# Kernel tuning notes

Hardware: AMD Instinct MI355X
Metric: run time of the kernel (lower is better)

The kernel has to match this reference:

```python
import jax, jax.numpy as jnp
import numpy as np

B, L, D = 256, 512, 768
ATTN_H, WIDTH_DIM = 1000, 20
BINS = jnp.array([1, 2, 3, 4, 5, 6, 7, 8, 12, 16, 20, 24, 32, 64, 128], dtype=jnp.int64)


def setup_inputs() -> dict:
    key = jax.random.key(0)
    ks = jax.random.split(key, 20)
    s = 0.02
    embeds = jax.random.normal(ks[0], (B, L, D), dtype=jnp.float32)
    spans = jnp.sort(jax.random.randint(ks[1], (B, 2), 0, L, dtype=jnp.int64), axis=1)
    inp = {
        "embeds": embeds,
        "spans": spans,
        # attention scorer: Linear(768,1000) -> LeakyReLU -> Linear(1000,1)
        "aw1": jax.random.normal(ks[2], (D, ATTN_H), dtype=jnp.float32) * s,
        "ab1": jnp.zeros((ATTN_H,), dtype=jnp.float32),
        "aw2": jax.random.normal(ks[3], (ATTN_H, 1), dtype=jnp.float32) * s,
        "ab2": jnp.zeros((1,), dtype=jnp.float32),
        # width embedding: [len(bins)+1 = 16, 20]
        "width_emb": jax.random.normal(ks[4], (16, WIDTH_DIM), dtype=jnp.float32) * s,
        # score MLP: 2324 -> 1024 -> 512 -> 256 -> 30
        "sw1": jax.random.normal(ks[5], (2324, 1024), dtype=jnp.float32) * s,
        "sb1": jnp.zeros((1024,), dtype=jnp.float32),
        "sw2": jax.random.normal(ks[6], (1024, 512), dtype=jnp.float32) * s,
        "sb2": jnp.zeros((512,), dtype=jnp.float32),
        "sw3": jax.random.normal(ks[7], (512, 256), dtype=jnp.float32) * s,
        "sb3": jnp.zeros((256,), dtype=jnp.float32),
        "sw4": jax.random.normal(ks[8], (256, 30), dtype=jnp.float32) * s,
        "sb4": jnp.zeros((30,), dtype=jnp.float32),
    }
    return inp


def reference(embeds, spans, aw1, ab1, aw2, ab2, width_emb,
              sw1, sb1, sw2, sb2, sw3, sb3, sw4, sb4):
    b, l, d = embeds.shape
    start, end = spans[:, 0], spans[:, 1]

    # gather start/end token embeds -> [B, 2*D]
    se = jnp.take_along_axis(embeds, spans[:, :, None], axis=1).reshape(b, 2 * d)

    # attention logits over all tokens: Linear -> LeakyReLU -> Linear
    h = jax.nn.leaky_relu(embeds @ aw1 + ab1)          # [B, L, 1000]
    attns = (h @ aw2 + ab2)[..., 0]                     # [B, L]

    # ragged per-span softmax pooling, vectorized via masking (inclusive span)
    cols = jnp.arange(l, dtype=spans.dtype)[None, :]
    mask = (cols >= start[:, None]) & (cols <= end[:, None])
    w = jax.nn.softmax(jnp.where(mask, attns, jnp.float32(-1e30)), axis=1)
    w = w * mask.astype(w.dtype)
    attn_embeds = jnp.einsum("bl,bld->bd", w, embeds)   # [B, D]

    # width bucket embedding
    widths = end - start + 1
    idx = jnp.sum(widths[:, None] > BINS[None, :], axis=1)
    wemb = width_emb[idx]                                # [B, 20]

    x = jnp.concatenate([se, attn_embeds, wemb], axis=1)  # [B, 2324]
    x = jax.nn.leaky_relu(x @ sw1 + sb1)
    x = jax.nn.leaky_relu(x @ sw2 + sb2)
    x = jax.nn.leaky_relu(x @ sw3 + sb3)
    return x @ sw4 + sb4                                  # [B, 30]
```

## Files before the change

### kernel.cpp

```cpp
#include <hip/hip_runtime.h>
#include <hip/hip_bf16.h>

#define B_   256
#define L_   512
#define D_   768
#define H_   1000
#define NPAD 1024
#define XDIM 2324
#define MAXPOS (B_*L_)

typedef _Float16 half8 __attribute__((ext_vector_type(8)));
typedef float    f32x4 __attribute__((ext_vector_type(4)));

__global__ __launch_bounds__(256) void scan_kernel(const int* __restrict__ spans,
                                                   int* __restrict__ meta) {
    int b = threadIdx.x;
    int s = spans[2 * b], e = spans[2 * b + 1];
    s = min(max(s, 0), L_ - 1);
    e = min(max(e, s), L_ - 1);
    int w = e - s + 1;
    __shared__ int sw[256];
    sw[b] = w;
    __syncthreads();
    for (int d = 1; d < 256; d <<= 1) {
        int v = 0;
        if (b >= d) v = sw[b - d];
        __syncthreads();
        if (b >= d) sw[b] += v;
        __syncthreads();
    }
    meta[b]       = sw[b] - w;
    meta[256 + b] = s;
    meta[512 + b] = e;
    if (b == 255) meta[768] = sw[255];
}

__global__ __launch_bounds__(256) void pos_fill(const int* __restrict__ meta,
                                                int* __restrict__ pos_list) {
    int b = blockIdx.x;
    int off = meta[b], start = meta[256 + b], end = meta[512 + b];
    int w = end - start + 1;
    for (int i = threadIdx.x; i < w; i += blockDim.x)
        pos_list[off + i] = (b << 16) | (start + i);
}

__global__ __launch_bounds__(256) void transpose_w(const float* __restrict__ aw1,
                                                   _Float16* __restrict__ WbT) {
    int k0 = blockIdx.x * 32, n0 = blockIdx.y * 32;
    int tx = threadIdx.x & 31, ty = threadIdx.x >> 5;
    __shared__ float T[32][33];
#pragma unroll
    for (int it = 0; it < 4; it++) {
        int k = k0 + ty + 8 * it;
        int n = n0 + tx;
        T[ty + 8 * it][tx] = (n < H_) ? aw1[(size_t)k * H_ + n] : 0.f;
    }
    __syncthreads();
#pragma unroll
    for (int it = 0; it < 4; it++) {
        int n = n0 + ty + 8 * it;
        WbT[(size_t)n * D_ + k0 + tx] = (_Float16)T[tx][ty + 8 * it];
    }
}

#define BM   128
#define BN   256
#define BKT  32
#define NKST (D_ / BKT)

#define GLD_LDS16(gsrc, ldst) \
    __builtin_amdgcn_global_load_lds((const __attribute__((address_space(1))) void*)(gsrc), \
                                     (__attribute__((address_space(3))) void*)(ldst), 16, 0, 0)

__global__ __launch_bounds__(512, 4) void attn_gemm_v4(
    const float* __restrict__ embeds, const _Float16* __restrict__ WbT,
    const float* __restrict__ ab1, const float* __restrict__ aw2,
    const int* __restrict__ pos_list, const int* __restrict__ meta,
    float* __restrict__ attns) {
    int npos = meta[768];
    int m0 = blockIdx.x * BM;
    if (m0 >= npos) return;
    int n0 = blockIdx.y * BN;
    int t = threadIdx.x;
    int lane = t & 63, w = t >> 6;
    int q = lane >> 4, l15 = lane & 15;
    int wr = w >> 2, wc = w & 3;

    __shared__ alignas(16) _Float16 As[2][BM][BKT];
    __shared__ alignas(16) _Float16 Bs[2][BN * BKT];
    __shared__ unsigned rowoff[BM];

    if (t < BM) {
        unsigned off = 0;
        int m = m0 + t;
        if (m < npos) {
            int p = pos_list[m];
            off = (unsigned)((p >> 16) * (L_ * D_) + (p & 0xffff) * D_);
        }
        rowoff[t] = off;
    }
    __syncthreads();

    const int arow = t >> 2;
    const int acol = (t & 3) * 8;
    const float* aptr = embeds + rowoff[arow] + acol;

    const _Float16* bptr = WbT + (size_t)(n0 + (t >> 2)) * D_ + (t & 3) * 8;

    float4 ar0, ar1;
    auto loadA = [&](int k0) {
        const float* p = aptr + k0;
        ar0 = *(const float4*)(p + 0);
        ar1 = *(const float4*)(p + 4);
    };
    auto writeA = [&](int bbuf) {
        half8 h0;
        h0[0] = (_Float16)ar0.x; h0[1] = (_Float16)ar0.y;
        h0[2] = (_Float16)ar0.z; h0[3] = (_Float16)ar0.w;
        h0[4] = (_Float16)ar1.x; h0[5] = (_Float16)ar1.y;
        h0[6] = (_Float16)ar1.z; h0[7] = (_Float16)ar1.w;
        *(half8*)&As[bbuf][arow][acol] = h0;
    };
    auto issueB = [&](int bbuf, int k0) {
        const _Float16* s0 = bptr + k0;
        _Float16* d0 = &Bs[bbuf][0] + w * 512;
        GLD_LDS16(s0, d0);
        const _Float16* s1 = s0 + (size_t)128 * D_;
        _Float16* d1 = d0 + 4096;
        GLD_LDS16(s1, d1);
    };

    f32x4 acc[4][4];
#pragma unroll
    for (int mi = 0; mi < 4; mi++)
#pragma unroll
        for (int ni = 0; ni < 4; ni++) acc[mi][ni] = (f32x4){0.f, 0.f, 0.f, 0.f};

    auto compute = [&](int bbuf) {
        half8 af[4], bf[4];
#pragma unroll
        for (int mi = 0; mi < 4; mi++)
            af[mi] = *(const half8*)&As[bbuf][wr * 64 + mi * 16 + l15][q * 8];
#pragma unroll
        for (int ni = 0; ni < 4; ni++)
            bf[ni] = *(const half8*)&Bs[bbuf][((wc * 64 + ni * 16 + l15) << 5) + q * 8];
#pragma unroll
        for (int mi = 0; mi < 4; mi++)
#pragma unroll
            for (int ni = 0; ni < 4; ni++)
                acc[mi][ni] = __builtin_amdgcn_mfma_f32_16x16x32_f16(
                    af[mi], bf[ni], acc[mi][ni], 0, 0, 0);
    };

    issueB(0, 0);
    loadA(0);
    writeA(0);
    __syncthreads();

    int buf = 0;
#pragma unroll 2
    for (int ks = 0; ks < NKST - 1; ks++) {
        int kn = (ks + 1) * BKT;
        issueB(buf ^ 1, kn);
        loadA(kn);
        compute(buf);
        writeA(buf ^ 1);
        __syncthreads();
        buf ^= 1;
    }
    compute(buf);

    int colb = n0 + wc * 64;
    float bj[4], aj[4];
#pragma unroll
    for (int ni = 0; ni < 4; ni++) {
        int col = colb + ni * 16 + l15;
        bool v = col < H_;
        bj[ni] = v ? ab1[col] : 0.f;
        aj[ni] = v ? aw2[col] : 0.f;
    }
#pragma unroll
    for (int mi = 0; mi < 4; mi++) {
#pragma unroll
        for (int r = 0; r < 4; r++) {
            float p = 0.f;
#pragma unroll
            for (int ni = 0; ni < 4; ni++) {
                float h = acc[mi][ni][r] + bj[ni];
                h = h > 0.f ? h : 0.01f * h;
                p += h * aj[ni];
            }
            p += __shfl_xor(p, 1);
            p += __shfl_xor(p, 2);
            p += __shfl_xor(p, 4);
            p += __shfl_xor(p, 8);
            if (l15 == 0) {
                int row = m0 + wr * 64 + mi * 16 + q * 4 + r;
                if (row < npos) atomicAdd(&attns[row], p);
            }
        }
    }
}

__global__ __launch_bounds__(256) void build_x(
    const float* __restrict__ embeds, const float* __restrict__ attns,
    const int* __restrict__ meta, const float* __restrict__ width_emb,
    float* __restrict__ x) {
    int b = blockIdx.x, s = blockIdx.y, t = threadIdx.x;
    int off = meta[b], start = meta[256 + b], end = meta[512 + b];
    int w = end - start + 1;
    __shared__ float sv[512];
    __shared__ float red[256];
    for (int i = t; i < w; i += 256) sv[i] = attns[off + i];
    __syncthreads();
    float m = -3.0e38f;
    for (int i = t; i < w; i += 256) m = fmaxf(m, sv[i]);
    red[t] = m;
    __syncthreads();
    for (int st = 128; st > 0; st >>= 1) {
        if (t < st) red[t] = fmaxf(red[t], red[t + st]);
        __syncthreads();
    }
    float mx = red[0];
    __syncthreads();
    float ssum = 0.f;
    for (int i = t; i < w; i += 256) {
        float e = __expf(sv[i] - mx);
        sv[i] = e;
        ssum += e;
    }
    red[t] = ssum;
    __syncthreads();
    for (int st = 128; st > 0; st >>= 1) {
        if (t < st) red[t] += red[t + st];
        __syncthreads();
    }
    float inv = 1.0f / red[0];
    __syncthreads();

    int dim = s * 256 + t;
    const float* base = embeds + ((size_t)b * L_ + start) * D_ + dim;
    float acc = 0.f;
    int i = 0;
    for (; i + 3 < w; i += 4) {
        float w0 = sv[i], w1 = sv[i + 1], w2 = sv[i + 2], w3 = sv[i + 3];
        const float* p = base + (size_t)i * D_;
        acc += w0 * p[0] + w1 * p[D_] + w2 * p[2 * D_] + w3 * p[3 * D_];
    }
    for (; i < w; i++) acc += sv[i] * base[(size_t)i * D_];

    float* xb = x + (size_t)b * XDIM;
    xb[1536 + dim] = acc * inv;
    xb[dim]        = base[0];
    xb[768 + dim]  = embeds[((size_t)b * L_ + end) * D_ + dim];
    if (s == 0 && t < 20) {
        const int bins[15] = {1, 2, 3, 4, 5, 6, 7, 8, 12, 16, 20, 24, 32, 64, 128};
        int idx = 0;
#pragma unroll
        for (int q2 = 0; q2 < 15; q2++) idx += (w > bins[q2]);
        xb[2304 + t] = width_emb[idx * 20 + t];
    }
}

__global__ __launch_bounds__(256) void mlp_gemm_sk(
    const float* __restrict__ A, const float* __restrict__ abias, int aleaky,
    const float* __restrict__ W, float* __restrict__ out,
    int M, int N, int K, int kchunk) {
    __shared__ float As[16][68];
    __shared__ float Ws[16][64];
    int t = threadIdx.x;
    int tx = t & 15, ty = t >> 4;
    int m0 = blockIdx.x * 64, n0 = blockIdx.y * 64;
    int ks = blockIdx.z * kchunk;
    int ke = min(ks + kchunk, K);
    if (ks >= ke) return;
    int ar = t >> 2, akc = (t & 3) * 4;
    int wk = t >> 4, wnc = (t & 15) * 4;
    bool n4 = ((N & 3) == 0);

    float acc[4][4];
#pragma unroll
    for (int i = 0; i < 4; i++)
#pragma unroll
        for (int j = 0; j < 4; j++) acc[i][j] = 0.f;

    auto loadA = [&](int k0) -> float4 {
        float4 r = make_float4(0.f, 0.f, 0.f, 0.f);
        int k = k0 + akc;
        if (k < ke) {
            r = *(const float4*)(A + (size_t)(m0 + ar) * K + k);
            if (abias) {
                r.x += abias[k];     r.y += abias[k + 1];
                r.z += abias[k + 2]; r.w += abias[k + 3];
                if (aleaky) {
                    r.x = r.x > 0.f ? r.x : 0.01f * r.x;
                    r.y = r.y > 0.f ? r.y : 0.01f * r.y;
                    r.z = r.z > 0.f ? r.z : 0.01f * r.z;
                    r.w = r.w > 0.f ? r.w : 0.01f * r.w;
                }
            }
        }
        return r;
    };
    auto loadW = [&](int k0) -> float4 {
        float4 r = make_float4(0.f, 0.f, 0.f, 0.f);
        int k = k0 + wk;
        if (k < ke) {
            int n = n0 + wnc;
            const float* p = W + (size_t)k * N + n;
            if (n4) {
                r = *(const float4*)p;
            } else {
                float tmp[4];
#pragma unroll
                for (int q2 = 0; q2 < 4; q2++)
                    tmp[q2] = (n + q2 < N) ? p[q2] : 0.f;
                r = make_float4(tmp[0], tmp[1], tmp[2], tmp[3]);
            }
        }
        return r;
    };

    float4 aR = loadA(ks), wR = loadW(ks);
    for (int k0 = ks; k0 < ke; k0 += 16) {
        As[akc + 0][ar] = aR.x;
        As[akc + 1][ar] = aR.y;
        As[akc + 2][ar] = aR.z;
        As[akc + 3][ar] = aR.w;
        *(float4*)&Ws[wk][wnc] = wR;
        __syncthreads();
        if (k0 + 16 < ke) { aR = loadA(k0 + 16); wR = loadW(k0 + 16); }
#pragma unroll
        for (int kk = 0; kk < 16; kk++) {
            float4 a = *(const float4*)&As[kk][ty * 4];
            float4 b = *(const float4*)&Ws[kk][tx * 4];
            float av[4] = {a.x, a.y, a.z, a.w};
            float bv[4] = {b.x, b.y, b.z, b.w};
#pragma unroll
            for (int i = 0; i < 4; i++)
#pragma unroll
                for (int j = 0; j < 4; j++) acc[i][j] += av[i] * bv[j];
        }
        __syncthreads();
    }
#pragma unroll
    for (int i = 0; i < 4; i++) {
#pragma unroll
        for (int j = 0; j < 4; j++) {
            int nn = n0 + tx * 4 + j;
            if (nn < N)
                atomicAdd(&out[(size_t)(m0 + ty * 4 + i) * N + nn], acc[i][j]);
        }
    }
}

__global__ __launch_bounds__(256) void bias_act(
    const float* __restrict__ src, const float* __restrict__ bias,
    float* __restrict__ dst, int total, int N, int leaky) {
    int i = blockIdx.x * 256 + threadIdx.x;
    int stride = gridDim.x * 256;
    for (; i < total; i += stride) {
        float v = src[i] + bias[i % N];
        if (leaky) v = v > 0.f ? v : 0.01f * v;
        dst[i] = v;
    }
}

extern "C" void kernel_launch(void* const* d_in, const int* in_sizes, int n_in,
                              void* d_out, int out_size, void* d_ws, size_t ws_size,
                              hipStream_t stream) {
    const float* embeds    = (const float*)d_in[0];
    const int*   spans     = (const int*)d_in[1];
    const float* aw1       = (const float*)d_in[2];
    const float* ab1       = (const float*)d_in[3];
    const float* aw2       = (const float*)d_in[4];
    const float* width_emb = (const float*)d_in[6];
    const float* sw1 = (const float*)d_in[7],  *sb1 = (const float*)d_in[8];
    const float* sw2 = (const float*)d_in[9],  *sb2 = (const float*)d_in[10];
    const float* sw3 = (const float*)d_in[11], *sb3 = (const float*)d_in[12];
    const float* sw4 = (const float*)d_in[13], *sb4 = (const float*)d_in[14];
    float* out = (float*)d_out;

    char* ws = (char*)d_ws;
    float*     attns    = (float*)ws;
    int*       pos_list = (int*)(ws + (size_t)MAXPOS * 4);
    int*       meta     = (int*)(ws + (size_t)MAXPOS * 8);
    _Float16*  WbT      = (_Float16*)(ws + (size_t)MAXPOS * 8 + 4096);
    float* x  = (float*)(ws + (size_t)MAXPOS * 8 + 4096 + (size_t)NPAD * D_ * 2);
    float* y1 = x + (size_t)B_ * XDIM;
    float* y2 = y1 + (size_t)B_ * 1024;
    float* y3 = y2 + (size_t)B_ * 512;
    float* y4 = y3 + (size_t)B_ * 256;
    size_t ybytes = ((size_t)B_ * (1024 + 512 + 256 + 30)) * 4;

    hipMemsetAsync(y1, 0, ybytes, stream);
    hipMemsetAsync(attns, 0, (size_t)MAXPOS * 4, stream);
    scan_kernel<<<1, 256, 0, stream>>>(spans, meta);
    pos_fill<<<B_, 256, 0, stream>>>(meta, pos_list);
    transpose_w<<<dim3(D_ / 32, NPAD / 32), 256, 0, stream>>>(aw1, WbT);
    attn_gemm_v4<<<dim3(MAXPOS / BM, NPAD / BN), 512, 0, stream>>>(
        embeds, WbT, ab1, aw2, pos_list, meta, attns);
    build_x<<<dim3(B_, 3), 256, 0, stream>>>(embeds, attns, meta, width_emb, x);

    mlp_gemm_sk<<<dim3(4, 16, 8), 256, 0, stream>>>(x,  nullptr, 0, sw1, y1, B_, 1024, XDIM, 292);
    mlp_gemm_sk<<<dim3(4, 8, 8), 256, 0, stream>>>(y1, sb1, 1, sw2, y2, B_, 512, 1024, 128);
    mlp_gemm_sk<<<dim3(4, 4, 8), 256, 0, stream>>>(y2, sb2, 1, sw3, y3, B_, 256, 512, 64);
    mlp_gemm_sk<<<dim3(4, 1, 8), 256, 0, stream>>>(y3, sb3, 1, sw4, y4, B_, 30, 256, 32);
    bias_act<<<30, 256, 0, stream>>>(y4, sb4, out, B_ * 30, 30, 0);
}
```

Before: 731.1 us.

## Pre-gather span rows to fp16 buffer and load A tiles directly into LDS

Adds a separate kernel that gathers the in-span token rows from embeds, converts them to fp16 and writes them to a contiguous buffer. The attention GEMM then streams A tiles with global_load_lds like B, dropping the register round-trip and the in-loop fp32-to-fp16 conversion. The grid is also swapped so the four N-blocks sharing an M tile are adjacent, which may improve reuse of A in cache. The cost is an extra kernel launch and a write plus re-read of an fp16 copy of the gathered rows. Any A rows past npos in the last tile are read from uninitialized workspace.

```diff
diff --git a/kernel.cpp b/kernel.cpp
--- a/kernel.cpp
+++ b/kernel.cpp
@@ -63,6 +63,28 @@
     }
 }
 
+__global__ __launch_bounds__(256) void gather_a16(
+    const float* __restrict__ embeds, const int* __restrict__ pos_list,
+    const int* __restrict__ meta, _Float16* __restrict__ Af16) {
+    int npos = meta[768];
+    int total = npos * 96;
+    for (int cid = blockIdx.x * 256 + threadIdx.x; cid < total;
+         cid += gridDim.x * 256) {
+        int row = cid / 96, c8 = (cid % 96) * 8;
+        int p = pos_list[row];
+        const float* src = embeds + (size_t)(p >> 16) * (L_ * D_)
+                                  + (size_t)(p & 0xffff) * D_ + c8;
+        float4 v0 = *(const float4*)src;
+        float4 v1 = *(const float4*)(src + 4);
+        half8 h;
+        h[0] = (_Float16)v0.x; h[1] = (_Float16)v0.y;
+        h[2] = (_Float16)v0.z; h[3] = (_Float16)v0.w;
+        h[4] = (_Float16)v1.x; h[5] = (_Float16)v1.y;
+        h[6] = (_Float16)v1.z; h[7] = (_Float16)v1.w;
+        *(half8*)&Af16[(size_t)row * D_ + c8] = h;
+    }
+}
+
 #define BM   128
 #define BN   256
 #define BKT  32
@@ -72,15 +94,14 @@
     __builtin_amdgcn_global_load_lds((const __attribute__((address_space(1))) void*)(gsrc), \
                                      (__attribute__((address_space(3))) void*)(ldst), 16, 0, 0)
 
-__global__ __launch_bounds__(512, 4) void attn_gemm_v4(
-    const float* __restrict__ embeds, const _Float16* __restrict__ WbT,
+__global__ __launch_bounds__(512, 4) void attn_gemm_v5(
+    const _Float16* __restrict__ Af16, const _Float16* __restrict__ WbT,
     const float* __restrict__ ab1, const float* __restrict__ aw2,
-    const int* __restrict__ pos_list, const int* __restrict__ meta,
-    float* __restrict__ attns) {
+    const int* __restrict__ meta, float* __restrict__ attns) {
     int npos = meta[768];
-    int m0 = blockIdx.x * BM;
+    int m0 = blockIdx.y * BM;
     if (m0 >= npos) return;
-    int n0 = blockIdx.y * BN;
+    int n0 = blockIdx.x * BN;
     int t = threadIdx.x;
     int lane = t & 63, w = t >> 6;
     int q = lane >> 4, l15 = lane & 15;
@@ -88,38 +109,13 @@
 
     __shared__ alignas(16) _Float16 As[2][BM][BKT];
     __shared__ alignas(16) _Float16 Bs[2][BN * BKT];
-    __shared__ unsigned rowoff[BM];
-
-    if (t < BM) {
-        unsigned off = 0;
-        int m = m0 + t;
-        if (m < npos) {
-            int p = pos_list[m];
-            off = (unsigned)((p >> 16) * (L_ * D_) + (p & 0xffff) * D_);
-        }
-        rowoff[t] = off;
-    }
-    __syncthreads();
-
-    const int arow = t >> 2;
-    const int acol = (t & 3) * 8;
-    const float* aptr = embeds + rowoff[arow] + acol;
-
+
+    const _Float16* aptr = Af16 + (size_t)(m0 + (t >> 2)) * D_ + (t & 3) * 8;
     const _Float16* bptr = WbT + (size_t)(n0 + (t >> 2)) * D_ + (t & 3) * 8;
 
-    float4 ar0, ar1;
-    auto loadA = [&](int k0) {
-        const float* p = aptr + k0;
-        ar0 = *(const float4*)(p + 0);
-        ar1 = *(const float4*)(p + 4);
-    };
-    auto writeA = [&](int bbuf) {
-        half8 h0;
-        h0[0] = (_Float16)ar0.x; h0[1] = (_Float16)ar0.y;
-        h0[2] = (_Float16)ar0.z; h0[3] = (_Float16)ar0.w;
-        h0[4] = (_Float16)ar1.x; h0[5] = (_Float16)ar1.y;
-        h0[6] = (_Float16)ar1.z; h0[7] = (_Float16)ar1.w;
-        *(half8*)&As[bbuf][arow][acol] = h0;
+    auto issueA = [&](int bbuf, int k0) {
+        _Float16* d = (_Float16*)As[bbuf] + w * 512;
+        GLD_LDS16(aptr + k0, d);
     };
     auto issueB = [&](int bbuf, int k0) {
         const _Float16* s0 = bptr + k0;
@@ -152,19 +148,17 @@
                     af[mi], bf[ni], acc[mi][ni], 0, 0, 0);
     };
 
+    issueA(0, 0);
     issueB(0, 0);
-    loadA(0);
-    writeA(0);
     __syncthreads();
 
     int buf = 0;
 #pragma unroll 2
     for (int ks = 0; ks < NKST - 1; ks++) {
         int kn = (ks + 1) * BKT;
+        issueA(buf ^ 1, kn);
         issueB(buf ^ 1, kn);
-        loadA(kn);
         compute(buf);
-        writeA(buf ^ 1);
         __syncthreads();
         buf ^= 1;
     }
@@ -391,6 +385,7 @@
     float* y2 = y1 + (size_t)B_ * 1024;
     float* y3 = y2 + (size_t)B_ * 512;
     float* y4 = y3 + (size_t)B_ * 256;
+    _Float16* Af16 = (_Float16*)(y4 + (size_t)B_ * 30 + 64);
     size_t ybytes = ((size_t)B_ * (1024 + 512 + 256 + 30)) * 4;
 
     hipMemsetAsync(y1, 0, ybytes, stream);
@@ -398,8 +393,9 @@
     scan_kernel<<<1, 256, 0, stream>>>(spans, meta);
     pos_fill<<<B_, 256, 0, stream>>>(meta, pos_list);
     transpose_w<<<dim3(D_ / 32, NPAD / 32), 256, 0, stream>>>(aw1, WbT);
-    attn_gemm_v4<<<dim3(MAXPOS / BM, NPAD / BN), 512, 0, stream>>>(
-        embeds, WbT, ab1, aw2, pos_list, meta, attns);
+    gather_a16<<<2048, 256, 0, stream>>>(embeds, pos_list, meta, Af16);
+    attn_gemm_v5<<<dim3(NPAD / BN, MAXPOS / BM), 512, 0, stream>>>(
+        Af16, WbT, ab1, aw2, meta, attns);
     build_x<<<dim3(B_, 3), 256, 0, stream>>>(embeds, attns, meta, width_emb, x);
 
     mlp_gemm_sk<<<dim3(4, 16, 8), 256, 0, stream>>>(x,  nullptr, 0, sw1, y1, B_, 1024, XDIM, 292);
```

Result: slower. 747.1 us (+2.2%).

## Loop over all hidden columns per block in attention GEMM, removing atomics

Applied to the files above, without the earlier changes.

The attention-score GEMM now gives each 256-thread block 64 gathered rows and loops over all four 256-column groups of the hidden dimension. Partial scores build up in registers and a shared-memory reduction, then go to attns with one plain store per row. This removes the cross-block atomicAdd and the memset of attns. The cost is that each block re-reads the embed rows for every column group, and the grid has one dimension with smaller tiles, which may lower reuse of the weight tile and MFMA density per block.

```diff
diff --git a/kernel.cpp b/kernel.cpp
--- a/kernel.cpp
+++ b/kernel.cpp
@@ -63,34 +63,30 @@
     }
 }
 
-#define BM   128
-#define BN   256
 #define BKT  32
-#define NKST (D_ / BKT)
 
 #define GLD_LDS16(gsrc, ldst) \
     __builtin_amdgcn_global_load_lds((const __attribute__((address_space(1))) void*)(gsrc), \
                                      (__attribute__((address_space(3))) void*)(ldst), 16, 0, 0)
 
-__global__ __launch_bounds__(512, 4) void attn_gemm_v4(
+__global__ __launch_bounds__(256, 3) void attn_gemm_v6(
     const float* __restrict__ embeds, const _Float16* __restrict__ WbT,
     const float* __restrict__ ab1, const float* __restrict__ aw2,
     const int* __restrict__ pos_list, const int* __restrict__ meta,
     float* __restrict__ attns) {
     int npos = meta[768];
-    int m0 = blockIdx.x * BM;
+    int m0 = blockIdx.x * 64;
     if (m0 >= npos) return;
-    int n0 = blockIdx.y * BN;
     int t = threadIdx.x;
     int lane = t & 63, w = t >> 6;
     int q = lane >> 4, l15 = lane & 15;
-    int wr = w >> 2, wc = w & 3;
-
-    __shared__ alignas(16) _Float16 As[2][BM][BKT];
-    __shared__ alignas(16) _Float16 Bs[2][BN * BKT];
-    __shared__ unsigned rowoff[BM];
-
-    if (t < BM) {
+
+    __shared__ alignas(16) _Float16 As[2][64][BKT];
+    __shared__ alignas(16) _Float16 Bs[2][256 * BKT];
+    __shared__ float attns_s[4][64];
+    __shared__ unsigned rowoff[64];
+
+    if (t < 64) {
         unsigned off = 0;
         int m = m0 + t;
         if (m < npos) {
@@ -101,49 +97,52 @@
     }
     __syncthreads();
 
-    const int arow = t >> 2;
-    const int acol = (t & 3) * 8;
+    const int arow = t >> 2, acol = (t & 3) * 8;
     const float* aptr = embeds + rowoff[arow] + acol;
-
-    const _Float16* bptr = WbT + (size_t)(n0 + (t >> 2)) * D_ + (t & 3) * 8;
+    const _Float16* bbase = WbT + (size_t)(t >> 2) * D_ + (t & 3) * 8;
 
     float4 ar0, ar1;
     auto loadA = [&](int k0) {
-        const float* p = aptr + k0;
-        ar0 = *(const float4*)(p + 0);
-        ar1 = *(const float4*)(p + 4);
-    };
-    auto writeA = [&](int bbuf) {
-        half8 h0;
-        h0[0] = (_Float16)ar0.x; h0[1] = (_Float16)ar0.y;
-        h0[2] = (_Float16)ar0.z; h0[3] = (_Float16)ar0.w;
-        h0[4] = (_Float16)ar1.x; h0[5] = (_Float16)ar1.y;
-        h0[6] = (_Float16)ar1.z; h0[7] = (_Float16)ar1.w;
-        *(half8*)&As[bbuf][arow][acol] = h0;
-    };
-    auto issueB = [&](int bbuf, int k0) {
-        const _Float16* s0 = bptr + k0;
-        _Float16* d0 = &Bs[bbuf][0] + w * 512;
-        GLD_LDS16(s0, d0);
-        const _Float16* s1 = s0 + (size_t)128 * D_;
-        _Float16* d1 = d0 + 4096;
-        GLD_LDS16(s1, d1);
+        ar0 = *(const float4*)(aptr + k0);
+        ar1 = *(const float4*)(aptr + k0 + 4);
+    };
+    auto writeA = [&](int b) {
+        half8 h;
+        h[0] = (_Float16)ar0.x; h[1] = (_Float16)ar0.y;
+        h[2] = (_Float16)ar0.z; h[3] = (_Float16)ar0.w;
+        h[4] = (_Float16)ar1.x; h[5] = (_Float16)ar1.y;
+        h[6] = (_Float16)ar1.z; h[7] = (_Float16)ar1.w;
+        *(half8*)&As[b][arow][acol] = h;
+    };
+    auto issueB = [&](int b, int g, int k0) {
+#pragma unroll
+        for (int j = 0; j < 4; j++) {
+            const _Float16* s = bbase + (size_t)(g * 256 + j * 64) * D_ + k0;
+            _Float16* d = &Bs[b][0] + j * 2048 + w * 512;
+            GLD_LDS16(s, d);
+        }
     };
 
     f32x4 acc[4][4];
+    float pacc[4][4];
 #pragma unroll
     for (int mi = 0; mi < 4; mi++)
 #pragma unroll
-        for (int ni = 0; ni < 4; ni++) acc[mi][ni] = (f32x4){0.f, 0.f, 0.f, 0.f};
-
-    auto compute = [&](int bbuf) {
+        for (int ni = 0; ni < 4; ni++) {
+            acc[mi][ni] = (f32x4){0.f, 0.f, 0.f, 0.f};
+            pacc[mi][ni] = 0.f;
+        }
+
+    auto compute = [&](int b) {
         half8 af[4], bf[4];
 #pragma unroll
         for (int mi = 0; mi < 4; mi++)
-            af[mi] = *(const half8*)&As[bbuf][wr * 64 + mi * 16 + l15][q * 8];
-#pragma unroll
-        for (int ni = 0; ni < 4; ni++)
-            bf[ni] = *(const half8*)&Bs[bbuf][((wc * 64 + ni * 16 + l15) << 5) + q * 8];
+            af[mi] = *(const half8*)&As[b][mi * 16 + l15][q * 8];
+#pragma unroll
+        for (int ni = 0; ni < 4; ni++) {
+            int col = w * 64 + ni * 16 + l15;
+            bf[ni] = *(const half8*)&Bs[b][(col << 5) + q * 8];
+        }
 #pragma unroll
         for (int mi = 0; mi < 4; mi++)
 #pragma unroll
@@ -152,54 +151,69 @@
                     af[mi], bf[ni], acc[mi][ni], 0, 0, 0);
     };
 
-    issueB(0, 0);
+    issueB(0, 0, 0);
     loadA(0);
     writeA(0);
     __syncthreads();
 
     int buf = 0;
-#pragma unroll 2
-    for (int ks = 0; ks < NKST - 1; ks++) {
-        int kn = (ks + 1) * BKT;
-        issueB(buf ^ 1, kn);
-        loadA(kn);
-        compute(buf);
-        writeA(buf ^ 1);
-        __syncthreads();
-        buf ^= 1;
-    }
-    compute(buf);
-
-    int colb = n0 + wc * 64;
-    float bj[4], aj[4];
-#pragma unroll
-    for (int ni = 0; ni < 4; ni++) {
-        int col = colb + ni * 16 + l15;
-        bool v = col < H_;
-        bj[ni] = v ? ab1[col] : 0.f;
-        aj[ni] = v ? aw2[col] : 0.f;
-    }
-#pragma unroll
-    for (int mi = 0; mi < 4; mi++) {
-#pragma unroll
-        for (int r = 0; r < 4; r++) {
-            float p = 0.f;
-#pragma unroll
-            for (int ni = 0; ni < 4; ni++) {
-                float h = acc[mi][ni][r] + bj[ni];
-                h = h > 0.f ? h : 0.01f * h;
-                p += h * aj[ni];
+    for (int g = 0; g < 4; g++) {
+        for (int kk = 0; kk < 24; kk++) {
+            int g1 = (kk == 23) ? g + 1 : g;
+            int k1 = (kk == 23) ? 0 : (kk + 1) * BKT;
+            bool pf = (g1 < 4);
+            if (pf) {
+                issueB(buf ^ 1, g1, k1);
+                loadA(k1);
             }
-            p += __shfl_xor(p, 1);
-            p += __shfl_xor(p, 2);
-            p += __shfl_xor(p, 4);
-            p += __shfl_xor(p, 8);
-            if (l15 == 0) {
-                int row = m0 + wr * 64 + mi * 16 + q * 4 + r;
-                if (row < npos) atomicAdd(&attns[row], p);
+            compute(buf);
+            if (pf) writeA(buf ^ 1);
+            __syncthreads();
+            buf ^= 1;
+        }
+        float bj[4], aj[4];
+#pragma unroll
+        for (int ni = 0; ni < 4; ni++) {
+            int col = g * 256 + w * 64 + ni * 16 + l15;
+            bool v = col < H_;
+            bj[ni] = v ? ab1[col] : 0.f;
+            aj[ni] = v ? aw2[col] : 0.f;
+        }
+#pragma unroll
+        for (int mi = 0; mi < 4; mi++) {
+#pragma unroll
+            for (int r = 0; r < 4; r++) {
+                float p = 0.f;
+#pragma unroll
+                for (int ni = 0; ni < 4; ni++) {
+                    float h = acc[mi][ni][r] + bj[ni];
+                    h = h > 0.f ? h : 0.01f * h;
+                    p += h * aj[ni];
+                }
+                p += __shfl_xor(p, 1);
+                p += __shfl_xor(p, 2);
+                p += __shfl_xor(p, 4);
+                p += __shfl_xor(p, 8);
+                pacc[mi][r] += p;
             }
         }
-    }
+#pragma unroll
+        for (int mi = 0; mi < 4; mi++)
+#pragma unroll
+            for (int ni = 0; ni < 4; ni++)
+                acc[mi][ni] = (f32x4){0.f, 0.f, 0.f, 0.f};
+    }
+
+    if (l15 == 0) {
+#pragma unroll
+        for (int mi = 0; mi < 4; mi++)
+#pragma unroll
+            for (int r = 0; r < 4; r++)
+                attns_s[w][mi * 16 + q * 4 + r] = pacc[mi][r];
+    }
+    __syncthreads();
+    if (t < 64 && m0 + t < npos)
+        attns[m0 + t] = attns_s[0][t] + attns_s[1][t] + attns_s[2][t] + attns_s[3][t];
 }
 
 __global__ __launch_bounds__(256) void build_x(
@@ -394,11 +408,10 @@
     size_t ybytes = ((size_t)B_ * (1024 + 512 + 256 + 30)) * 4;
 
     hipMemsetAsync(y1, 0, ybytes, stream);
-    hipMemsetAsync(attns, 0, (size_t)MAXPOS * 4, stream);
     scan_kernel<<<1, 256, 0, stream>>>(spans, meta);
     pos_fill<<<B_, 256, 0, stream>>>(meta, pos_list);
     transpose_w<<<dim3(D_ / 32, NPAD / 32), 256, 0, stream>>>(aw1, WbT);
-    attn_gemm_v4<<<dim3(MAXPOS / BM, NPAD / BN), 512, 0, stream>>>(
+    attn_gemm_v6<<<MAXPOS / 64, 256, 0, stream>>>(
         embeds, WbT, ab1, aw2, pos_list, meta, attns);
     build_x<<<dim3(B_, 3), 256, 0, stream>>>(embeds, attns, meta, width_emb, x);
 
```

New measurement: 762.5 us. +4.3%, slower.
